# Optimization experiments

Hardware: AMD Instinct MI355X
Metric: run time of the kernel (lower is better)

Reference implementation:

```python
import jax, jax.numpy as jnp
import numpy as np

T, B, I, H, L = 512, 256, 128, 256, 2

def _gru_layer(x, W_ih, W_hh, b_ih, b_hh):
    # x: [T, B, in], W_ih: [3H, in], W_hh: [3H, H], biases: [3H]
    # PyTorch gate order: r, z, n
    Hd = W_hh.shape[1]
    gi = jnp.einsum('tbi,gi->tbg', x, W_ih) + b_ih  # precompute input gates [T,B,3H]

    def step(h, gi_t):
        gh = h @ W_hh.T + b_hh
        i_r, i_z, i_n = jnp.split(gi_t, 3, axis=-1)
        h_r, h_z, h_n = jnp.split(gh, 3, axis=-1)
        r = jax.nn.sigmoid(i_r + h_r)
        z = jax.nn.sigmoid(i_z + h_z)
        n = jnp.tanh(i_n + r * h_n)
        h_new = (1.0 - z) * n + z * h
        return h_new, h_new

    h0 = jnp.zeros((x.shape[1], Hd), dtype=x.dtype)
    _, hs = jax.lax.scan(step, h0, gi)
    return hs  # [T, B, H]

def setup_inputs() -> dict:
    key = jax.random.key(0)
    ks = jax.random.split(key, 11)
    s = 1.0 / np.sqrt(H)
    u = lambda k, shp: jax.random.uniform(k, shp, jnp.float32, -s, s)
    return {
        'x': jax.random.normal(ks[0], (T, B, I), jnp.float32),
        'W_ih0': u(ks[1], (3 * H, I)),
        'W_hh0': u(ks[2], (3 * H, H)),
        'b_ih0': u(ks[3], (3 * H,)),
        'b_hh0': u(ks[4], (3 * H,)),
        'W_ih1': u(ks[5], (3 * H, H)),
        'W_hh1': u(ks[6], (3 * H, H)),
        'b_ih1': u(ks[7], (3 * H,)),
        'b_hh1': u(ks[8], (3 * H,)),
        'W_fc': u(ks[9], (H, H)),
        'b_fc': u(ks[10], (H,)),
    }

def reference(x, W_ih0, W_hh0, b_ih0, b_hh0, W_ih1, W_hh1, b_ih1, b_hh1, W_fc, b_fc):
    h1 = _gru_layer(x, W_ih0, W_hh0, b_ih0, b_hh0)   # [T,B,H]
    h2 = _gru_layer(h1, W_ih1, W_hh1, b_ih1, b_hh1)  # [T,B,H]
    last = h2[-1]                                    # [B,H] last timestep
    return last @ W_fc.T + b_fc
```

## Files before the change

kernel.cpp:

```cpp
#include <hip/hip_runtime.h>

#define TT 512
#define BB 256
#define II 128
#define HH 256
#define LDH 264

typedef __attribute__((ext_vector_type(8))) short short8;
typedef __attribute__((ext_vector_type(4))) float floatx4;
typedef __attribute__((ext_vector_type(4))) float fvec4;
typedef unsigned long long u64;

#define OFF_WIH0 0
#define OFF_WHH0 (OFF_WIH0 + 3 * HH * II)
#define OFF_WIH1 (OFF_WHH0 + 3 * HH * HH)
#define OFF_WHH1 (OFF_WIH1 + 3 * HH * HH)
#define W_TOTAL (OFF_WHH1 + 3 * HH * HH)
#define H1G_OFF W_TOTAL
#define H2G_OFF (H1G_OFF + 2 * BB * HH)
#define WS_SHORTS (H2G_OFF + 2 * BB * HH)
#define FLAGS_OFF_BYTES (WS_SHORTS * 2)
#define FLAG_STRIDE 32

__device__ __forceinline__ short f2bf(float f) {
  unsigned u = __builtin_bit_cast(unsigned, f);
  u = u + 0x7fffu + ((u >> 16) & 1u);
  return (short)(u >> 16);
}
__device__ __forceinline__ float fast_sigmoid(float x) {
  return __fdividef(1.0f, 1.0f + __expf(-x));
}
__device__ __forceinline__ float fast_tanh(float x) {
  return 1.0f - __fdividef(2.0f, 1.0f + __expf(2.0f * x));
}
__device__ __forceinline__ short8 cvt8(const float* __restrict__ p) {
  fvec4 lo = *(const fvec4*)p;
  fvec4 hi = *(const fvec4*)(p + 4);
  short8 r;
  r[0] = f2bf(lo[0]); r[1] = f2bf(lo[1]); r[2] = f2bf(lo[2]); r[3] = f2bf(lo[3]);
  r[4] = f2bf(hi[0]); r[5] = f2bf(hi[1]); r[6] = f2bf(hi[2]); r[7] = f2bf(hi[3]);
  return r;
}
__device__ __forceinline__ u64 ld_sc1(const u64* p) {
  return __hip_atomic_load(p, __ATOMIC_RELAXED, __HIP_MEMORY_SCOPE_AGENT);
}

__global__ __launch_bounds__(256) void cvt_weights(
    const float* __restrict__ w0, const float* __restrict__ w1,
    const float* __restrict__ w2, const float* __restrict__ w3,
    short* __restrict__ out) {
  int i = blockIdx.x * 256 + threadIdx.x;
  if (i >= W_TOTAL) return;
  float v;
  if (i < OFF_WHH0)      v = w0[i - OFF_WIH0];
  else if (i < OFF_WIH1) v = w1[i - OFF_WHH0];
  else if (i < OFF_WHH1) v = w2[i - OFF_WIH1];
  else                   v = w3[i - OFF_WHH1];
  out[i] = f2bf(v);
}

__global__ __launch_bounds__(256) void init_state(unsigned* __restrict__ hz,
                                                  unsigned* __restrict__ flags) {
  int i = blockIdx.x * 256 + threadIdx.x;
  if (i < 2 * BB * HH) hz[i] = 0u;
  if (i < 16 * FLAG_STRIDE) flags[i] = 0u;
}

__global__ __launch_bounds__(384) void gru_sync(
    const float* __restrict__ x, const short* __restrict__ wb,
    const float* __restrict__ bih0, const float* __restrict__ bhh0,
    const float* __restrict__ bih1, const float* __restrict__ bhh1,
    const float* __restrict__ Wfc, const float* __restrict__ bfc,
    short* __restrict__ h1g, short* __restrict__ h2g,
    unsigned* __restrict__ flags, float* __restrict__ out) {
  const int tid = threadIdx.x;
  const int lane = tid & 63;
  const int w = tid >> 6;
  const int quad = lane >> 4;
  const int col = lane & 15;
  const int bt = blockIdx.x & 15;
  const int ht = blockIdx.x >> 4;
  const int layer = w / 3, gate = w % 3;
  const int j = ht * 16 + col;

  __shared__ __align__(16) short ldsA[2][16][LDH];
  __shared__ __align__(16) float gt[2][6][16][20];

  const short* wih = wb + (layer ? OFF_WIH1 : OFF_WIH0);
  const short* whh = wb + (layer ? OFF_WHH1 : OFF_WHH0);
  short8 wfI[8], wfH[8];
  if (layer == 0) {
#pragma unroll
    for (int f = 0; f < 4; ++f)
      wfI[f] = *(const short8*)(wih + (gate * HH + j) * II + f * 32 + quad * 8);
#pragma unroll
    for (int f = 4; f < 8; ++f) wfI[f] = short8{0, 0, 0, 0, 0, 0, 0, 0};
  } else {
#pragma unroll
    for (int f = 0; f < 8; ++f)
      wfI[f] = *(const short8*)(wih + (gate * HH + j) * HH + f * 32 + quad * 8);
  }
#pragma unroll
  for (int f = 0; f < 8; ++f)
    wfH[f] = *(const short8*)(whh + (gate * HH + j) * HH + f * 32 + quad * 8);

  const float* bihL = layer ? bih1 : bih0;
  const float* bhhL = layer ? bhh1 : bhh0;
  float bI, bH;
  if (gate == 2) { bI = bihL[2 * HH + j]; bH = bhhL[2 * HH + j]; }
  else { bI = bihL[gate * HH + j] + bhhL[gate * HH + j]; bH = 0.f; }

  float h1a = 0.f, h1b = 0.f, h2a = 0.f, h2b = 0.f;
  const int r1 = tid >> 3, c1 = (tid & 7) * 2;
  const int r2 = (tid - 256) >> 3, c2 = ((tid - 256) & 7) * 2;

  unsigned* cnt = flags + bt * FLAG_STRIDE;
  const size_t tbase = (size_t)(bt * 16) * HH;

  for (int p = 0; p <= TT; ++p) {
    short8 ax[4];
    if (w < 3 && p < TT) {
      const float* xr = x + ((size_t)p * BB + bt * 16 + col) * II + quad * 8;
#pragma unroll
      for (int f = 0; f < 4; ++f) ax[f] = cvt8(xr + f * 32);
    }

    if (p > 0) {
      if (tid == 0) {
        unsigned tgt = 16u * (unsigned)p;
        int guard = 0;
        while (__hip_atomic_load(cnt, __ATOMIC_RELAXED,
                                 __HIP_MEMORY_SCOPE_AGENT) < tgt &&
               guard < (1 << 20))
          ++guard;
      }
      __syncthreads();
    }

    {
      const u64* s1 = (const u64*)(h1g + ((p + 1) & 1) * BB * HH + tbase);
      const u64* s2 = (const u64*)(h2g + (p & 1) * BB * HH + tbase);
      u64* d1 = (u64*)&ldsA[0][0][0];
      u64* d2 = (u64*)&ldsA[1][0][0];
      if (tid < 256) {
#pragma unroll
        for (int q = 0; q < 4; ++q) {
          int i = tid * 4 + q, row = i >> 6, c = i & 63;
          d1[row * (LDH / 4) + c] = ld_sc1(s1 + i);
        }
      }
      if (tid >= 128) {
        int t2 = tid - 128;
#pragma unroll
        for (int q = 0; q < 4; ++q) {
          int i = t2 * 4 + q, row = i >> 6, c = i & 63;
          d2[row * (LDH / 4) + c] = ld_sc1(s2 + i);
        }
      }
    }
    __syncthreads();

    floatx4 aI = floatx4{bI, bI, bI, bI};
    floatx4 aH = floatx4{bH, bH, bH, bH};
    const short* a1 = &ldsA[0][col][0];
    const short* a2 = &ldsA[1][col][0];
    if (layer == 0) {
      if (p < TT) {
#pragma unroll
        for (int f = 0; f < 4; ++f)
          aI = __builtin_amdgcn_mfma_f32_16x16x32_bf16(ax[f], wfI[f], aI, 0, 0, 0);
      }
#pragma unroll
      for (int f = 0; f < 8; ++f) {
        short8 a = *(const short8*)(a1 + f * 32 + quad * 8);
        aH = __builtin_amdgcn_mfma_f32_16x16x32_bf16(a, wfH[f], aH, 0, 0, 0);
      }
    } else {
#pragma unroll
      for (int f = 0; f < 8; ++f) {
        short8 a = *(const short8*)(a1 + f * 32 + quad * 8);
        aI = __builtin_amdgcn_mfma_f32_16x16x32_bf16(a, wfI[f], aI, 0, 0, 0);
      }
#pragma unroll
      for (int f = 0; f < 8; ++f) {
        short8 a = *(const short8*)(a2 + f * 32 + quad * 8);
        aH = __builtin_amdgcn_mfma_f32_16x16x32_bf16(a, wfH[f], aH, 0, 0, 0);
      }
    }
#pragma unroll
    for (int i = 0; i < 4; ++i) {
      gt[0][w][quad * 4 + i][col] = aI[i];
      gt[1][w][quad * 4 + i][col] = aH[i];
    }
    __syncthreads();

    if (tid < 128 && p < TT) {
      float rA = fast_sigmoid(gt[0][0][r1][c1] + gt[1][0][r1][c1]);
      float zA = fast_sigmoid(gt[0][1][r1][c1] + gt[1][1][r1][c1]);
      float nA = fast_tanh(gt[0][2][r1][c1] + rA * gt[1][2][r1][c1]);
      h1a = nA + zA * (h1a - nA);
      float rB = fast_sigmoid(gt[0][0][r1][c1 + 1] + gt[1][0][r1][c1 + 1]);
      float zB = fast_sigmoid(gt[0][1][r1][c1 + 1] + gt[1][1][r1][c1 + 1]);
      float nB = fast_tanh(gt[0][2][r1][c1 + 1] + rB * gt[1][2][r1][c1 + 1]);
      h1b = nB + zB * (h1b - nB);
      unsigned val = ((unsigned)(unsigned short)f2bf(h1b) << 16) |
                     (unsigned)(unsigned short)f2bf(h1a);
      unsigned* dst = (unsigned*)(h1g + (p & 1) * BB * HH +
                                  (bt * 16 + r1) * HH + ht * 16 + c1);
      __hip_atomic_store(dst, val, __ATOMIC_RELAXED, __HIP_MEMORY_SCOPE_AGENT);
    }
    if (tid >= 256 && p > 0) {
      float rA = fast_sigmoid(gt[0][3][r2][c2] + gt[1][3][r2][c2]);
      float zA = fast_sigmoid(gt[0][4][r2][c2] + gt[1][4][r2][c2]);
      float nA = fast_tanh(gt[0][5][r2][c2] + rA * gt[1][5][r2][c2]);
      h2a = nA + zA * (h2a - nA);
      float rB = fast_sigmoid(gt[0][3][r2][c2 + 1] + gt[1][3][r2][c2 + 1]);
      float zB = fast_sigmoid(gt[0][4][r2][c2 + 1] + gt[1][4][r2][c2 + 1]);
      float nB = fast_tanh(gt[0][5][r2][c2 + 1] + rB * gt[1][5][r2][c2 + 1]);
      h2b = nB + zB * (h2b - nB);
      unsigned val = ((unsigned)(unsigned short)f2bf(h2b) << 16) |
                     (unsigned)(unsigned short)f2bf(h2a);
      unsigned* dst = (unsigned*)(h2g + ((p + 1) & 1) * BB * HH +
                                  (bt * 16 + r2) * HH + ht * 16 + c2);
      __hip_atomic_store(dst, val, __ATOMIC_RELAXED, __HIP_MEMORY_SCOPE_AGENT);
    }
    __syncthreads();
    if (tid == 0)
      __hip_atomic_fetch_add(cnt, 1u, __ATOMIC_RELAXED,
                             __HIP_MEMORY_SCOPE_AGENT);
  }

  if (tid == 0) {
    unsigned tgt = 16u * (unsigned)(TT + 1);
    int guard = 0;
    while (__hip_atomic_load(cnt, __ATOMIC_RELAXED, __HIP_MEMORY_SCOPE_AGENT) <
               tgt &&
           guard < (1 << 20))
      ++guard;
  }
  __syncthreads();
  {
    const u64* s1 = (const u64*)(h2g + 1 * BB * HH + tbase);
    u64* d1 = (u64*)&ldsA[0][0][0];
    if (tid < 256) {
#pragma unroll
      for (int q = 0; q < 4; ++q) {
        int i = tid * 4 + q, row = i >> 6, c = i & 63;
        d1[row * (LDH / 4) + c] = ld_sc1(s1 + i);
      }
    }
  }
  __syncthreads();
  if (w == 0) {
    float bbv = bfc[j];
    floatx4 acc = floatx4{bbv, bbv, bbv, bbv};
#pragma unroll
    for (int f = 0; f < 8; ++f) {
      short8 a = *(const short8*)(&ldsA[0][col][0] + f * 32 + quad * 8);
      short8 bfrag = cvt8(Wfc + j * HH + f * 32 + quad * 8);
      acc = __builtin_amdgcn_mfma_f32_16x16x32_bf16(a, bfrag, acc, 0, 0, 0);
    }
#pragma unroll
    for (int i = 0; i < 4; ++i)
      out[(size_t)(bt * 16 + quad * 4 + i) * HH + j] = acc[i];
  }
}

extern "C" void kernel_launch(void* const* d_in, const int* in_sizes, int n_in,
                              void* d_out, int out_size, void* d_ws,
                              size_t ws_size, hipStream_t stream) {
  const float* x = (const float*)d_in[0];
  const float* Wih0 = (const float*)d_in[1];
  const float* Whh0 = (const float*)d_in[2];
  const float* bih0 = (const float*)d_in[3];
  const float* bhh0 = (const float*)d_in[4];
  const float* Wih1 = (const float*)d_in[5];
  const float* Whh1 = (const float*)d_in[6];
  const float* bih1 = (const float*)d_in[7];
  const float* bhh1 = (const float*)d_in[8];
  const float* Wfc = (const float*)d_in[9];
  const float* bfc = (const float*)d_in[10];

  short* wb = (short*)d_ws;
  short* h1g = wb + H1G_OFF;
  short* h2g = wb + H2G_OFF;
  unsigned* flags = (unsigned*)((char*)d_ws + FLAGS_OFF_BYTES);
  unsigned* hz = (unsigned*)(wb + H1G_OFF);

  cvt_weights<<<(W_TOTAL + 255) / 256, 256, 0, stream>>>(Wih0, Whh0, Wih1, Whh1, wb);
  init_state<<<(2 * BB * HH + 255) / 256, 256, 0, stream>>>(hz, flags);
  gru_sync<<<256, 384, 0, stream>>>(x, wb, bih0, bhh0, bih1, bhh1, Wfc, bfc,
                                    h1g, h2g, flags, (float*)d_out);
}
```

Before: 1.891 ms.

## Process two batch tiles per block to reuse register-held weights

```diff
diff --git a/kernel.cpp b/kernel.cpp
--- a/kernel.cpp
+++ b/kernel.cpp
@@ -78,13 +78,13 @@
   const int w = tid >> 6;
   const int quad = lane >> 4;
   const int col = lane & 15;
-  const int bt = blockIdx.x & 15;
-  const int ht = blockIdx.x >> 4;
+  const int q = blockIdx.x & 7;
+  const int ht = blockIdx.x >> 3;
   const int layer = w / 3, gate = w % 3;
   const int j = ht * 16 + col;
 
-  __shared__ __align__(16) short ldsA[2][16][LDH];
-  __shared__ __align__(16) float gt[2][6][16][20];
+  __shared__ __align__(16) short lds[2][2][16][LDH];
+  __shared__ __align__(16) float gt[2][2][6][16][20];
 
   const short* wih = wb + (layer ? OFF_WIH1 : OFF_WIH0);
   const short* whh = wb + (layer ? OFF_WHH1 : OFF_WHH0);
@@ -110,19 +110,25 @@
   if (gate == 2) { bI = bihL[2 * HH + j]; bH = bhhL[2 * HH + j]; }
   else { bI = bihL[gate * HH + j] + bhhL[gate * HH + j]; bH = 0.f; }
 
-  float h1a = 0.f, h1b = 0.f, h2a = 0.f, h2b = 0.f;
+  float h1aA = 0.f, h1bA = 0.f, h2aA = 0.f, h2bA = 0.f;
+  float h1aB = 0.f, h1bB = 0.f, h2aB = 0.f, h2bB = 0.f;
   const int r1 = tid >> 3, c1 = (tid & 7) * 2;
   const int r2 = (tid - 256) >> 3, c2 = ((tid - 256) & 7) * 2;
 
-  unsigned* cnt = flags + bt * FLAG_STRIDE;
-  const size_t tbase = (size_t)(bt * 16) * HH;
+  unsigned* cnt = flags + q * FLAG_STRIDE;
+  const size_t tbaseA = (size_t)(q * 16) * HH;
+  const size_t tbaseB = (size_t)((q + 8) * 16) * HH;
 
   for (int p = 0; p <= TT; ++p) {
-    short8 ax[4];
+    short8 axA[4], axB[4];
     if (w < 3 && p < TT) {
-      const float* xr = x + ((size_t)p * BB + bt * 16 + col) * II + quad * 8;
-#pragma unroll
-      for (int f = 0; f < 4; ++f) ax[f] = cvt8(xr + f * 32);
+      const float* xrA = x + ((size_t)p * BB + q * 16 + col) * II + quad * 8;
+      const float* xrB = xrA + (size_t)8 * 16 * II;
+#pragma unroll
+      for (int f = 0; f < 4; ++f) {
+        axA[f] = cvt8(xrA + f * 32);
+        axB[f] = cvt8(xrB + f * 32);
+      }
     }
 
     if (p > 0) {
@@ -138,91 +144,145 @@
     }
 
     {
-      const u64* s1 = (const u64*)(h1g + ((p + 1) & 1) * BB * HH + tbase);
-      const u64* s2 = (const u64*)(h2g + (p & 1) * BB * HH + tbase);
-      u64* d1 = (u64*)&ldsA[0][0][0];
-      u64* d2 = (u64*)&ldsA[1][0][0];
+      const u64* s1A = (const u64*)(h1g + ((p + 1) & 1) * BB * HH + tbaseA);
+      const u64* s2A = (const u64*)(h2g + (p & 1) * BB * HH + tbaseA);
+      const u64* s1B = (const u64*)(h1g + ((p + 1) & 1) * BB * HH + tbaseB);
+      const u64* s2B = (const u64*)(h2g + (p & 1) * BB * HH + tbaseB);
+      u64* d1A = (u64*)&lds[0][0][0][0];
+      u64* d2A = (u64*)&lds[0][1][0][0];
+      u64* d1B = (u64*)&lds[1][0][0][0];
+      u64* d2B = (u64*)&lds[1][1][0][0];
       if (tid < 256) {
 #pragma unroll
-        for (int q = 0; q < 4; ++q) {
-          int i = tid * 4 + q, row = i >> 6, c = i & 63;
-          d1[row * (LDH / 4) + c] = ld_sc1(s1 + i);
+        for (int qq = 0; qq < 4; ++qq) {
+          int i = tid * 4 + qq, row = i >> 6, c = i & 63;
+          d1A[row * (LDH / 4) + c] = ld_sc1(s1A + i);
+          d1B[row * (LDH / 4) + c] = ld_sc1(s1B + i);
         }
       }
       if (tid >= 128) {
         int t2 = tid - 128;
 #pragma unroll
-        for (int q = 0; q < 4; ++q) {
-          int i = t2 * 4 + q, row = i >> 6, c = i & 63;
-          d2[row * (LDH / 4) + c] = ld_sc1(s2 + i);
+        for (int qq = 0; qq < 4; ++qq) {
+          int i = t2 * 4 + qq, row = i >> 6, c = i & 63;
+          d2A[row * (LDH / 4) + c] = ld_sc1(s2A + i);
+          d2B[row * (LDH / 4) + c] = ld_sc1(s2B + i);
         }
       }
     }
     __syncthreads();
 
-    floatx4 aI = floatx4{bI, bI, bI, bI};
-    floatx4 aH = floatx4{bH, bH, bH, bH};
-    const short* a1 = &ldsA[0][col][0];
-    const short* a2 = &ldsA[1][col][0];
+    floatx4 aIA = floatx4{bI, bI, bI, bI};
+    floatx4 aHA = floatx4{bH, bH, bH, bH};
+    floatx4 aIB = floatx4{bI, bI, bI, bI};
+    floatx4 aHB = floatx4{bH, bH, bH, bH};
+    const short* a1A = &lds[0][0][col][0];
+    const short* a2A = &lds[0][1][col][0];
+    const short* a1B = &lds[1][0][col][0];
+    const short* a2B = &lds[1][1][col][0];
     if (layer == 0) {
       if (p < TT) {
 #pragma unroll
-        for (int f = 0; f < 4; ++f)
-          aI = __builtin_amdgcn_mfma_f32_16x16x32_bf16(ax[f], wfI[f], aI, 0, 0, 0);
+        for (int f = 0; f < 4; ++f) {
+          aIA = __builtin_amdgcn_mfma_f32_16x16x32_bf16(axA[f], wfI[f], aIA, 0, 0, 0);
+          aIB = __builtin_amdgcn_mfma_f32_16x16x32_bf16(axB[f], wfI[f], aIB, 0, 0, 0);
+        }
       }
 #pragma unroll
       for (int f = 0; f < 8; ++f) {
-        short8 a = *(const short8*)(a1 + f * 32 + quad * 8);
-        aH = __builtin_amdgcn_mfma_f32_16x16x32_bf16(a, wfH[f], aH, 0, 0, 0);
+        short8 aA = *(const short8*)(a1A + f * 32 + quad * 8);
+        short8 aB = *(const short8*)(a1B + f * 32 + quad * 8);
+        aHA = __builtin_amdgcn_mfma_f32_16x16x32_bf16(aA, wfH[f], aHA, 0, 0, 0);
+        aHB = __builtin_amdgcn_mfma_f32_16x16x32_bf16(aB, wfH[f], aHB, 0, 0, 0);
       }
     } else {
 #pragma unroll
       for (int f = 0; f < 8; ++f) {
-        short8 a = *(const short8*)(a1 + f * 32 + quad * 8);
-        aI = __builtin_amdgcn_mfma_f32_16x16x32_bf16(a, wfI[f], aI, 0, 0, 0);
+        short8 aA = *(const short8*)(a1A + f * 32 + quad * 8);
+        short8 aB = *(const short8*)(a1B + f * 32 + quad * 8);
+        aIA = __builtin_amdgcn_mfma_f32_16x16x32_bf16(aA, wfI[f], aIA, 0, 0, 0);
+        aIB = __builtin_amdgcn_mfma_f32_16x16x32_bf16(aB, wfI[f], aIB, 0, 0, 0);
       }
 #pragma unroll
       for (int f = 0; f < 8; ++f) {
-        short8 a = *(const short8*)(a2 + f * 32 + quad * 8);
-        aH = __builtin_amdgcn_mfma_f32_16x16x32_bf16(a, wfH[f], aH, 0, 0, 0);
+        short8 aA = *(const short8*)(a2A + f * 32 + quad * 8);
+        short8 aB = *(const short8*)(a2B + f * 32 + quad * 8);
+        aHA = __builtin_amdgcn_mfma_f32_16x16x32_bf16(aA, wfH[f], aHA, 0, 0, 0);
+        aHB = __builtin_amdgcn_mfma_f32_16x16x32_bf16(aB, wfH[f], aHB, 0, 0, 0);
       }
     }
 #pragma unroll
     for (int i = 0; i < 4; ++i) {
-      gt[0][w][quad * 4 + i][col] = aI[i];
-      gt[1][w][quad * 4 + i][col] = aH[i];
+      gt[0][0][w][quad * 4 + i][col] = aIA[i];
+      gt[0][1][w][quad * 4 + i][col] = aHA[i];
+      gt[1][0][w][quad * 4 + i][col] = aIB[i];
+      gt[1][1][w][quad * 4 + i][col] = aHB[i];
     }
     __syncthreads();
 
     if (tid < 128 && p < TT) {
-      float rA = fast_sigmoid(gt[0][0][r1][c1] + gt[1][0][r1][c1]);
-      float zA = fast_sigmoid(gt[0][1][r1][c1] + gt[1][1][r1][c1]);
-      float nA = fast_tanh(gt[0][2][r1][c1] + rA * gt[1][2][r1][c1]);
-      h1a = nA + zA * (h1a - nA);
-      float rB = fast_sigmoid(gt[0][0][r1][c1 + 1] + gt[1][0][r1][c1 + 1]);
-      float zB = fast_sigmoid(gt[0][1][r1][c1 + 1] + gt[1][1][r1][c1 + 1]);
-      float nB = fast_tanh(gt[0][2][r1][c1 + 1] + rB * gt[1][2][r1][c1 + 1]);
-      h1b = nB + zB * (h1b - nB);
-      unsigned val = ((unsigned)(unsigned short)f2bf(h1b) << 16) |
-                     (unsigned)(unsigned short)f2bf(h1a);
-      unsigned* dst = (unsigned*)(h1g + (p & 1) * BB * HH +
-                                  (bt * 16 + r1) * HH + ht * 16 + c1);
-      __hip_atomic_store(dst, val, __ATOMIC_RELAXED, __HIP_MEMORY_SCOPE_AGENT);
+      {
+        float rA = fast_sigmoid(gt[0][0][0][r1][c1] + gt[0][1][0][r1][c1]);
+        float zA = fast_sigmoid(gt[0][0][1][r1][c1] + gt[0][1][1][r1][c1]);
+        float nA = fast_tanh(gt[0][0][2][r1][c1] + rA * gt[0][1][2][r1][c1]);
+        h1aA = nA + zA * (h1aA - nA);
+        float rB = fast_sigmoid(gt[0][0][0][r1][c1 + 1] + gt[0][1][0][r1][c1 + 1]);
+        float zB = fast_sigmoid(gt[0][0][1][r1][c1 + 1] + gt[0][1][1][r1][c1 + 1]);
+        float nB = fast_tanh(gt[0][0][2][r1][c1 + 1] + rB * gt[0][1][2][r1][c1 + 1]);
+        h1bA = nB + zB * (h1bA - nB);
+        unsigned val = ((unsigned)(unsigned short)f2bf(h1bA) << 16) |
+                       (unsigned)(unsigned short)f2bf(h1aA);
+        unsigned* dst = (unsigned*)(h1g + (p & 1) * BB * HH +
+                                    (q * 16 + r1) * HH + ht * 16 + c1);
+        __hip_atomic_store(dst, val, __ATOMIC_RELAXED, __HIP_MEMORY_SCOPE_AGENT);
+      }
+      {
+        float rA = fast_sigmoid(gt[1][0][0][r1][c1] + gt[1][1][0][r1][c1]);
+        float zA = fast_sigmoid(gt[1][0][1][r1][c1] + gt[1][1][1][r1][c1]);
+        float nA = fast_tanh(gt[1][0][2][r1][c1] + rA * gt[1][1][2][r1][c1]);
+        h1aB = nA + zA * (h1aB - nA);
+        float rB = fast_sigmoid(gt[1][0][0][r1][c1 + 1] + gt[1][1][0][r1][c1 + 1]);
+        float zB = fast_sigmoid(gt[1][0][1][r1][c1 + 1] + gt[1][1][1][r1][c1 + 1]);
+        float nB = fast_tanh(gt[1][0][2][r1][c1 + 1] + rB * gt[1][1][2][r1][c1 + 1]);
+        h1bB = nB + zB * (h1bB - nB);
+        unsigned val = ((unsigned)(unsigned short)f2bf(h1bB) << 16) |
+                       (unsigned)(unsigned short)f2bf(h1aB);
+        unsigned* dst = (unsigned*)(h1g + (p & 1) * BB * HH +
+                                    ((q + 8) * 16 + r1) * HH + ht * 16 + c1);
+        __hip_atomic_store(dst, val, __ATOMIC_RELAXED, __HIP_MEMORY_SCOPE_AGENT);
+      }
     }
     if (tid >= 256 && p > 0) {
-      float rA = fast_sigmoid(gt[0][3][r2][c2] + gt[1][3][r2][c2]);
-      float zA = fast_sigmoid(gt[0][4][r2][c2] + gt[1][4][r2][c2]);
-      float nA = fast_tanh(gt[0][5][r2][c2] + rA * gt[1][5][r2][c2]);
-      h2a = nA + zA * (h2a - nA);
-      float rB = fast_sigmoid(gt[0][3][r2][c2 + 1] + gt[1][3][r2][c2 + 1]);
-      float zB = fast_sigmoid(gt[0][4][r2][c2 + 1] + gt[1][4][r2][c2 + 1]);
-      float nB = fast_tanh(gt[0][5][r2][c2 + 1] + rB * gt[1][5][r2][c2 + 1]);
-      h2b = nB + zB * (h2b - nB);
-      unsigned val = ((unsigned)(unsigned short)f2bf(h2b) << 16) |
-                     (unsigned)(unsigned short)f2bf(h2a);
-      unsigned* dst = (unsigned*)(h2g + ((p + 1) & 1) * BB * HH +
-                                  (bt * 16 + r2) * HH + ht * 16 + c2);
-      __hip_atomic_store(dst, val, __ATOMIC_RELAXED, __HIP_MEMORY_SCOPE_AGENT);
+      {
+        float rA = fast_sigmoid(gt[0][0][3][r2][c2] + gt[0][1][3][r2][c2]);
+        float zA = fast_sigmoid(gt[0][0][4][r2][c2] + gt[0][1][4][r2][c2]);
+        float nA = fast_tanh(gt[0][0][5][r2][c2] + rA * gt[0][1][5][r2][c2]);
+        h2aA = nA + zA * (h2aA - nA);
+        float rB = fast_sigmoid(gt[0][0][3][r2][c2 + 1] + gt[0][1][3][r2][c2 + 1]);
+        float zB = fast_sigmoid(gt[0][0][4][r2][c2 + 1] + gt[0][1][4][r2][c2 + 1]);
+        float nB = fast_tanh(gt[0][0][5][r2][c2 + 1] + rB * gt[0][1][5][r2][c2 + 1]);
+        h2bA = nB + zB * (h2bA - nB);
+        unsigned val = ((unsigned)(unsigned short)f2bf(h2bA) << 16) |
+                       (unsigned)(unsigned short)f2bf(h2aA);
+        unsigned* dst = (unsigned*)(h2g + ((p + 1) & 1) * BB * HH +
+                                    (q * 16 + r2) * HH + ht * 16 + c2);
+        __hip_atomic_store(dst, val, __ATOMIC_RELAXED, __HIP_MEMORY_SCOPE_AGENT);
+      }
+      {
+        float rA = fast_sigmoid(gt[1][0][3][r2][c2] + gt[1][1][3][r2][c2]);
+        float zA = fast_sigmoid(gt[1][0][4][r2][c2] + gt[1][1][4][r2][c2]);
+        float nA = fast_tanh(gt[1][0][5][r2][c2] + rA * gt[1][1][5][r2][c2]);
+        h2aB = nA + zA * (h2aB - nA);
+        float rB = fast_sigmoid(gt[1][0][3][r2][c2 + 1] + gt[1][1][3][r2][c2 + 1]);
+        float zB = fast_sigmoid(gt[1][0][4][r2][c2 + 1] + gt[1][1][4][r2][c2 + 1]);
+        float nB = fast_tanh(gt[1][0][5][r2][c2 + 1] + rB * gt[1][1][5][r2][c2 + 1]);
+        h2bB = nB + zB * (h2bB - nB);
+        unsigned val = ((unsigned)(unsigned short)f2bf(h2bB) << 16) |
+                       (unsigned)(unsigned short)f2bf(h2aB);
+        unsigned* dst = (unsigned*)(h2g + ((p + 1) & 1) * BB * HH +
+                                    ((q + 8) * 16 + r2) * HH + ht * 16 + c2);
+        __hip_atomic_store(dst, val, __ATOMIC_RELAXED, __HIP_MEMORY_SCOPE_AGENT);
+      }
     }
     __syncthreads();
     if (tid == 0)
@@ -240,29 +300,35 @@
   }
   __syncthreads();
   {
-    const u64* s1 = (const u64*)(h2g + 1 * BB * HH + tbase);
-    u64* d1 = (u64*)&ldsA[0][0][0];
+    const u64* sA = (const u64*)(h2g + 1 * BB * HH + tbaseA);
+    const u64* sB = (const u64*)(h2g + 1 * BB * HH + tbaseB);
+    u64* dA = (u64*)&lds[0][0][0][0];
+    u64* dB = (u64*)&lds[1][0][0][0];
     if (tid < 256) {
 #pragma unroll
-      for (int q = 0; q < 4; ++q) {
-        int i = tid * 4 + q, row = i >> 6, c = i & 63;
-        d1[row * (LDH / 4) + c] = ld_sc1(s1 + i);
+      for (int qq = 0; qq < 4; ++qq) {
+        int i = tid * 4 + qq, row = i >> 6, c = i & 63;
+        dA[row * (LDH / 4) + c] = ld_sc1(sA + i);
+        dB[row * (LDH / 4) + c] = ld_sc1(sB + i);
       }
     }
   }
   __syncthreads();
-  if (w == 0) {
+  if (w < 2) {
+    const int g = w;
+    const short* av = &lds[g][0][col][0];
     float bbv = bfc[j];
     floatx4 acc = floatx4{bbv, bbv, bbv, bbv};
 #pragma unroll
     for (int f = 0; f < 8; ++f) {
-      short8 a = *(const short8*)(&ldsA[0][col][0] + f * 32 + quad * 8);
+      short8 a = *(const short8*)(av + f * 32 + quad * 8);
       short8 bfrag = cvt8(Wfc + j * HH + f * 32 + quad * 8);
       acc = __builtin_amdgcn_mfma_f32_16x16x32_bf16(a, bfrag, acc, 0, 0, 0);
     }
+    const int brow = (g ? (q + 8) : q) * 16;
 #pragma unroll
     for (int i = 0; i < 4; ++i)
-      out[(size_t)(bt * 16 + quad * 4 + i) * HH + j] = acc[i];
+      out[(size_t)(brow + quad * 4 + i) * HH + j] = acc[i];
   }
 }
 
@@ -289,6 +355,6 @@
 
   cvt_weights<<<(W_TOTAL + 255) / 256, 256, 0, stream>>>(Wih0, Whh0, Wih1, Whh1, wb);
   init_state<<<(2 * BB * HH + 255) / 256, 256, 0, stream>>>(hz, flags);
-  gru_sync<<<256, 384, 0, stream>>>(x, wb, bih0, bhh0, bih1, bhh1, Wfc, bfc,
+  gru_sync<<<128, 384, 0, stream>>>(x, wb, bih0, bhh0, bih1, bhh1, Wfc, bfc,
                                     h1g, h2g, flags, (float*)d_out);
 }
```

Result: slower. 3.303 ms (+74.6%).

## Split GRU into single-wave blocks per layer with per-tile flag dataflow sync

Applied to the files above, without the earlier changes.

```diff
diff --git a/kernel.cpp b/kernel.cpp
--- a/kernel.cpp
+++ b/kernel.cpp
@@ -4,7 +4,6 @@
 #define BB 256
 #define II 128
 #define HH 256
-#define LDH 264
 
 typedef __attribute__((ext_vector_type(8))) short short8;
 typedef __attribute__((ext_vector_type(4))) float floatx4;
@@ -21,6 +20,9 @@
 #define WS_SHORTS (H2G_OFF + 2 * BB * HH)
 #define FLAGS_OFF_BYTES (WS_SHORTS * 2)
 #define FLAG_STRIDE 32
+#define HPARW (BB * HH / 4)
+
+struct U64x2 { u64 lo, hi; };
 
 __device__ __forceinline__ short f2bf(float f) {
   unsigned u = __builtin_bit_cast(unsigned, f);
@@ -44,6 +46,16 @@
 __device__ __forceinline__ u64 ld_sc1(const u64* p) {
   return __hip_atomic_load(p, __ATOMIC_RELAXED, __HIP_MEMORY_SCOPE_AGENT);
 }
+__device__ __forceinline__ unsigned ld_flag(const unsigned* p) {
+  return __hip_atomic_load(p, __ATOMIC_RELAXED, __HIP_MEMORY_SCOPE_AGENT);
+}
+__device__ __forceinline__ void st_flag(unsigned* p, unsigned v) {
+  __hip_atomic_store(p, v, __ATOMIC_RELAXED, __HIP_MEMORY_SCOPE_AGENT);
+}
+__device__ __forceinline__ void st_h(unsigned short* p, unsigned short v) {
+  __hip_atomic_store(p, v, __ATOMIC_RELAXED, __HIP_MEMORY_SCOPE_AGENT);
+}
+#define DRAIN_VMEM asm volatile("s_waitcnt vmcnt(0)" ::: "memory")
 
 __global__ __launch_bounds__(256) void cvt_weights(
     const float* __restrict__ w0, const float* __restrict__ w1,
@@ -63,200 +75,187 @@
                                                   unsigned* __restrict__ flags) {
   int i = blockIdx.x * 256 + threadIdx.x;
   if (i < 2 * BB * HH) hz[i] = 0u;
-  if (i < 16 * FLAG_STRIDE) flags[i] = 0u;
-}
-
-__global__ __launch_bounds__(384) void gru_sync(
+  if (i < 32 * FLAG_STRIDE) flags[i] = 0u;
+}
+
+__global__ __launch_bounds__(64) void gru_sync(
     const float* __restrict__ x, const short* __restrict__ wb,
     const float* __restrict__ bih0, const float* __restrict__ bhh0,
     const float* __restrict__ bih1, const float* __restrict__ bhh1,
     const float* __restrict__ Wfc, const float* __restrict__ bfc,
     short* __restrict__ h1g, short* __restrict__ h2g,
     unsigned* __restrict__ flags, float* __restrict__ out) {
-  const int tid = threadIdx.x;
-  const int lane = tid & 63;
-  const int w = tid >> 6;
+  const int lane = threadIdx.x;
   const int quad = lane >> 4;
   const int col = lane & 15;
-  const int bt = blockIdx.x & 15;
-  const int ht = blockIdx.x >> 4;
-  const int layer = w / 3, gate = w % 3;
+  const int bid = blockIdx.x;
+  const int layer = bid >> 8;
+  const int bt = (bid >> 4) & 15;
+  const int ht = bid & 15;
   const int j = ht * 16 + col;
 
-  __shared__ __align__(16) short ldsA[2][16][LDH];
-  __shared__ __align__(16) float gt[2][6][16][20];
+  unsigned* h1fl = flags + bt * FLAG_STRIDE;
+  unsigned* h2fl = flags + (16 + bt) * FLAG_STRIDE;
+  unsigned* myfl = layer ? h2fl : h1fl;
 
   const short* wih = wb + (layer ? OFF_WIH1 : OFF_WIH0);
   const short* whh = wb + (layer ? OFF_WHH1 : OFF_WHH0);
-  short8 wfI[8], wfH[8];
-  if (layer == 0) {
-#pragma unroll
-    for (int f = 0; f < 4; ++f)
-      wfI[f] = *(const short8*)(wih + (gate * HH + j) * II + f * 32 + quad * 8);
-#pragma unroll
-    for (int f = 4; f < 8; ++f) wfI[f] = short8{0, 0, 0, 0, 0, 0, 0, 0};
-  } else {
-#pragma unroll
-    for (int f = 0; f < 8; ++f)
-      wfI[f] = *(const short8*)(wih + (gate * HH + j) * HH + f * 32 + quad * 8);
+  const int KI = layer ? HH : II;
+  short8 wI0[8], wI1[8], wI2[8], wH0[8], wH1[8], wH2[8];
+#pragma unroll
+  for (int f = 0; f < 8; ++f) {
+    if (f * 32 < KI) {
+      wI0[f] = *(const short8*)(wih + (0 * HH + j) * KI + f * 32 + quad * 8);
+      wI1[f] = *(const short8*)(wih + (1 * HH + j) * KI + f * 32 + quad * 8);
+      wI2[f] = *(const short8*)(wih + (2 * HH + j) * KI + f * 32 + quad * 8);
+    } else {
+      wI0[f] = short8{0,0,0,0,0,0,0,0};
+      wI1[f] = short8{0,0,0,0,0,0,0,0};
+      wI2[f] = short8{0,0,0,0,0,0,0,0};
+    }
+    wH0[f] = *(const short8*)(whh + (0 * HH + j) * HH + f * 32 + quad * 8);
+    wH1[f] = *(const short8*)(whh + (1 * HH + j) * HH + f * 32 + quad * 8);
+    wH2[f] = *(const short8*)(whh + (2 * HH + j) * HH + f * 32 + quad * 8);
   }
-#pragma unroll
-  for (int f = 0; f < 8; ++f)
-    wfH[f] = *(const short8*)(whh + (gate * HH + j) * HH + f * 32 + quad * 8);
-
   const float* bihL = layer ? bih1 : bih0;
   const float* bhhL = layer ? bhh1 : bhh0;
-  float bI, bH;
-  if (gate == 2) { bI = bihL[2 * HH + j]; bH = bhhL[2 * HH + j]; }
-  else { bI = bihL[gate * HH + j] + bhhL[gate * HH + j]; bH = 0.f; }
-
-  float h1a = 0.f, h1b = 0.f, h2a = 0.f, h2b = 0.f;
-  const int r1 = tid >> 3, c1 = (tid & 7) * 2;
-  const int r2 = (tid - 256) >> 3, c2 = ((tid - 256) & 7) * 2;
-
-  unsigned* cnt = flags + bt * FLAG_STRIDE;
-  const size_t tbase = (size_t)(bt * 16) * HH;
-
-  for (int p = 0; p <= TT; ++p) {
+  const float bI0 = bihL[j] + bhhL[j];
+  const float bI1 = bihL[HH + j] + bhhL[HH + j];
+  const float bI2 = bihL[2 * HH + j];
+  const float bH2 = bhhL[2 * HH + j];
+
+  float hprev0 = 0.f, hprev1 = 0.f, hprev2 = 0.f, hprev3 = 0.f;
+
+  const u64* h1w = (const u64*)h1g;
+  const u64* h2w = (const u64*)h2g;
+  const int rowW = (bt * 16 + col) * 64;
+
+  for (int p = 0; p < TT; ++p) {
     short8 ax[4];
-    if (w < 3 && p < TT) {
+    if (layer == 0) {
       const float* xr = x + ((size_t)p * BB + bt * 16 + col) * II + quad * 8;
 #pragma unroll
       for (int f = 0; f < 4; ++f) ax[f] = cvt8(xr + f * 32);
     }
 
-    if (p > 0) {
-      if (tid == 0) {
-        unsigned tgt = 16u * (unsigned)p;
+    {
+      unsigned tgt = 0;
+      const unsigned* fp = h1fl;
+      if (layer == 0) {
+        if (lane < 16)      { tgt = (unsigned)p; fp = h1fl + lane; }
+        else if (lane < 32) { tgt = (p >= 1) ? (unsigned)(p - 1) : 0u; fp = h2fl + (lane - 16); }
+      } else {
+        if (lane < 16)      { tgt = (unsigned)p; fp = h2fl + lane; }
+        else if (lane < 32) { tgt = (unsigned)(p + 1); fp = h1fl + (lane - 16); }
+      }
+      if (layer == 1 || p > 0) {
         int guard = 0;
-        while (__hip_atomic_load(cnt, __ATOMIC_RELAXED,
-                                 __HIP_MEMORY_SCOPE_AGENT) < tgt &&
-               guard < (1 << 20))
-          ++guard;
-      }
-      __syncthreads();
-    }
-
+        for (;;) {
+          unsigned v = ld_flag(fp);
+          if (__all(v >= tgt) || ++guard > (1 << 20)) break;
+        }
+      }
+    }
+
+    short8 a1[8], a2[8];
+    if (layer == 0) {
+      const u64* s1 = h1w + ((p + 1) & 1) * HPARW + rowW;
+#pragma unroll
+      for (int f = 0; f < 8; ++f) {
+        u64 lo = ld_sc1(s1 + f * 8 + quad * 2);
+        u64 hi = ld_sc1(s1 + f * 8 + quad * 2 + 1);
+        a1[f] = __builtin_bit_cast(short8, U64x2{lo, hi});
+      }
+    } else {
+      const u64* s1 = h1w + (p & 1) * HPARW + rowW;
+      const u64* s2 = h2w + ((p + 1) & 1) * HPARW + rowW;
+#pragma unroll
+      for (int f = 0; f < 8; ++f) {
+        u64 lo = ld_sc1(s1 + f * 8 + quad * 2);
+        u64 hi = ld_sc1(s1 + f * 8 + quad * 2 + 1);
+        a1[f] = __builtin_bit_cast(short8, U64x2{lo, hi});
+      }
+#pragma unroll
+      for (int f = 0; f < 8; ++f) {
+        u64 lo = ld_sc1(s2 + f * 8 + quad * 2);
+        u64 hi = ld_sc1(s2 + f * 8 + quad * 2 + 1);
+        a2[f] = __builtin_bit_cast(short8, U64x2{lo, hi});
+      }
+    }
+
+    floatx4 aR = floatx4{bI0, bI0, bI0, bI0};
+    floatx4 aZ = floatx4{bI1, bI1, bI1, bI1};
+    floatx4 aN = floatx4{bI2, bI2, bI2, bI2};
+    floatx4 hN = floatx4{bH2, bH2, bH2, bH2};
+    if (layer == 0) {
+#pragma unroll
+      for (int f = 0; f < 4; ++f) {
+        aR = __builtin_amdgcn_mfma_f32_16x16x32_bf16(ax[f], wI0[f], aR, 0, 0, 0);
+        aZ = __builtin_amdgcn_mfma_f32_16x16x32_bf16(ax[f], wI1[f], aZ, 0, 0, 0);
+        aN = __builtin_amdgcn_mfma_f32_16x16x32_bf16(ax[f], wI2[f], aN, 0, 0, 0);
+      }
+#pragma unroll
+      for (int f = 0; f < 8; ++f) {
+        aR = __builtin_amdgcn_mfma_f32_16x16x32_bf16(a1[f], wH0[f], aR, 0, 0, 0);
+        aZ = __builtin_amdgcn_mfma_f32_16x16x32_bf16(a1[f], wH1[f], aZ, 0, 0, 0);
+        hN = __builtin_amdgcn_mfma_f32_16x16x32_bf16(a1[f], wH2[f], hN, 0, 0, 0);
+      }
+    } else {
+#pragma unroll
+      for (int f = 0; f < 8; ++f) {
+        aR = __builtin_amdgcn_mfma_f32_16x16x32_bf16(a1[f], wI0[f], aR, 0, 0, 0);
+        aZ = __builtin_amdgcn_mfma_f32_16x16x32_bf16(a1[f], wI1[f], aZ, 0, 0, 0);
+        aN = __builtin_amdgcn_mfma_f32_16x16x32_bf16(a1[f], wI2[f], aN, 0, 0, 0);
+      }
+#pragma unroll
+      for (int f = 0; f < 8; ++f) {
+        aR = __builtin_amdgcn_mfma_f32_16x16x32_bf16(a2[f], wH0[f], aR, 0, 0, 0);
+        aZ = __builtin_amdgcn_mfma_f32_16x16x32_bf16(a2[f], wH1[f], aZ, 0, 0, 0);
+        hN = __builtin_amdgcn_mfma_f32_16x16x32_bf16(a2[f], wH2[f], hN, 0, 0, 0);
+      }
+    }
+
+    short* hout = (layer ? h2g : h1g) + (p & 1) * BB * HH;
+    unsigned short* dst = (unsigned short*)hout +
+                          (size_t)(bt * 16 + quad * 4) * HH + j;
     {
-      const u64* s1 = (const u64*)(h1g + ((p + 1) & 1) * BB * HH + tbase);
-      const u64* s2 = (const u64*)(h2g + (p & 1) * BB * HH + tbase);
-      u64* d1 = (u64*)&ldsA[0][0][0];
-      u64* d2 = (u64*)&ldsA[1][0][0];
-      if (tid < 256) {
-#pragma unroll
-        for (int q = 0; q < 4; ++q) {
-          int i = tid * 4 + q, row = i >> 6, c = i & 63;
-          d1[row * (LDH / 4) + c] = ld_sc1(s1 + i);
-        }
-      }
-      if (tid >= 128) {
-        int t2 = tid - 128;
-#pragma unroll
-        for (int q = 0; q < 4; ++q) {
-          int i = t2 * 4 + q, row = i >> 6, c = i & 63;
-          d2[row * (LDH / 4) + c] = ld_sc1(s2 + i);
-        }
-      }
-    }
-    __syncthreads();
-
-    floatx4 aI = floatx4{bI, bI, bI, bI};
-    floatx4 aH = floatx4{bH, bH, bH, bH};
-    const short* a1 = &ldsA[0][col][0];
-    const short* a2 = &ldsA[1][col][0];
-    if (layer == 0) {
-      if (p < TT) {
-#pragma unroll
-        for (int f = 0; f < 4; ++f)
-          aI = __builtin_amdgcn_mfma_f32_16x16x32_bf16(ax[f], wfI[f], aI, 0, 0, 0);
-      }
-#pragma unroll
-      for (int f = 0; f < 8; ++f) {
-        short8 a = *(const short8*)(a1 + f * 32 + quad * 8);
-        aH = __builtin_amdgcn_mfma_f32_16x16x32_bf16(a, wfH[f], aH, 0, 0, 0);
-      }
-    } else {
-#pragma unroll
-      for (int f = 0; f < 8; ++f) {
-        short8 a = *(const short8*)(a1 + f * 32 + quad * 8);
-        aI = __builtin_amdgcn_mfma_f32_16x16x32_bf16(a, wfI[f], aI, 0, 0, 0);
-      }
-#pragma unroll
-      for (int f = 0; f < 8; ++f) {
-        short8 a = *(const short8*)(a2 + f * 32 + quad * 8);
-        aH = __builtin_amdgcn_mfma_f32_16x16x32_bf16(a, wfH[f], aH, 0, 0, 0);
-      }
-    }
-#pragma unroll
-    for (int i = 0; i < 4; ++i) {
-      gt[0][w][quad * 4 + i][col] = aI[i];
-      gt[1][w][quad * 4 + i][col] = aH[i];
-    }
-    __syncthreads();
-
-    if (tid < 128 && p < TT) {
-      float rA = fast_sigmoid(gt[0][0][r1][c1] + gt[1][0][r1][c1]);
-      float zA = fast_sigmoid(gt[0][1][r1][c1] + gt[1][1][r1][c1]);
-      float nA = fast_tanh(gt[0][2][r1][c1] + rA * gt[1][2][r1][c1]);
-      h1a = nA + zA * (h1a - nA);
-      float rB = fast_sigmoid(gt[0][0][r1][c1 + 1] + gt[1][0][r1][c1 + 1]);
-      float zB = fast_sigmoid(gt[0][1][r1][c1 + 1] + gt[1][1][r1][c1 + 1]);
-      float nB = fast_tanh(gt[0][2][r1][c1 + 1] + rB * gt[1][2][r1][c1 + 1]);
-      h1b = nB + zB * (h1b - nB);
-      unsigned val = ((unsigned)(unsigned short)f2bf(h1b) << 16) |
-                     (unsigned)(unsigned short)f2bf(h1a);
-      unsigned* dst = (unsigned*)(h1g + (p & 1) * BB * HH +
-                                  (bt * 16 + r1) * HH + ht * 16 + c1);
-      __hip_atomic_store(dst, val, __ATOMIC_RELAXED, __HIP_MEMORY_SCOPE_AGENT);
-    }
-    if (tid >= 256 && p > 0) {
-      float rA = fast_sigmoid(gt[0][3][r2][c2] + gt[1][3][r2][c2]);
-      float zA = fast_sigmoid(gt[0][4][r2][c2] + gt[1][4][r2][c2]);
-      float nA = fast_tanh(gt[0][5][r2][c2] + rA * gt[1][5][r2][c2]);
-      h2a = nA + zA * (h2a - nA);
-      float rB = fast_sigmoid(gt[0][3][r2][c2 + 1] + gt[1][3][r2][c2 + 1]);
-      float zB = fast_sigmoid(gt[0][4][r2][c2 + 1] + gt[1][4][r2][c2 + 1]);
-      float nB = fast_tanh(gt[0][5][r2][c2 + 1] + rB * gt[1][5][r2][c2 + 1]);
-      h2b = nB + zB * (h2b - nB);
-      unsigned val = ((unsigned)(unsigned short)f2bf(h2b) << 16) |
-                     (unsigned)(unsigned short)f2bf(h2a);
-      unsigned* dst = (unsigned*)(h2g + ((p + 1) & 1) * BB * HH +
-                                  (bt * 16 + r2) * HH + ht * 16 + c2);
-      __hip_atomic_store(dst, val, __ATOMIC_RELAXED, __HIP_MEMORY_SCOPE_AGENT);
-    }
-    __syncthreads();
-    if (tid == 0)
-      __hip_atomic_fetch_add(cnt, 1u, __ATOMIC_RELAXED,
-                             __HIP_MEMORY_SCOPE_AGENT);
+      float r0 = fast_sigmoid(aR[0]), z0 = fast_sigmoid(aZ[0]);
+      float n0 = fast_tanh(aN[0] + r0 * hN[0]);
+      hprev0 = n0 + z0 * (hprev0 - n0);
+      st_h(dst + 0 * HH, (unsigned short)f2bf(hprev0));
+      float r1 = fast_sigmoid(aR[1]), z1 = fast_sigmoid(aZ[1]);
+      float n1 = fast_tanh(aN[1] + r1 * hN[1]);
+      hprev1 = n1 + z1 * (hprev1 - n1);
+      st_h(dst + 1 * HH, (unsigned short)f2bf(hprev1));
+      float r2 = fast_sigmoid(aR[2]), z2 = fast_sigmoid(aZ[2]);
+      float n2 = fast_tanh(aN[2] + r2 * hN[2]);
+      hprev2 = n2 + z2 * (hprev2 - n2);
+      st_h(dst + 2 * HH, (unsigned short)f2bf(hprev2));
+      float r3 = fast_sigmoid(aR[3]), z3 = fast_sigmoid(aZ[3]);
+      float n3 = fast_tanh(aN[3] + r3 * hN[3]);
+      hprev3 = n3 + z3 * (hprev3 - n3);
+      st_h(dst + 3 * HH, (unsigned short)f2bf(hprev3));
+    }
+    DRAIN_VMEM;
+    if (lane == 0) st_flag(myfl + ht, (unsigned)(p + 1));
   }
 
-  if (tid == 0) {
-    unsigned tgt = 16u * (unsigned)(TT + 1);
-    int guard = 0;
-    while (__hip_atomic_load(cnt, __ATOMIC_RELAXED, __HIP_MEMORY_SCOPE_AGENT) <
-               tgt &&
-           guard < (1 << 20))
-      ++guard;
-  }
-  __syncthreads();
-  {
-    const u64* s1 = (const u64*)(h2g + 1 * BB * HH + tbase);
-    u64* d1 = (u64*)&ldsA[0][0][0];
-    if (tid < 256) {
-#pragma unroll
-      for (int q = 0; q < 4; ++q) {
-        int i = tid * 4 + q, row = i >> 6, c = i & 63;
-        d1[row * (LDH / 4) + c] = ld_sc1(s1 + i);
-      }
-    }
-  }
-  __syncthreads();
-  if (w == 0) {
+  if (layer == 1) {
+    {
+      int guard = 0;
+      for (;;) {
+        unsigned v = (lane < 16) ? ld_flag(h2fl + lane) : (unsigned)TT;
+        if (__all(v >= (unsigned)TT) || ++guard > (1 << 20)) break;
+      }
+    }
+    const u64* s2 = h2w + ((TT - 1) & 1) * HPARW + rowW;
     float bbv = bfc[j];
     floatx4 acc = floatx4{bbv, bbv, bbv, bbv};
 #pragma unroll
     for (int f = 0; f < 8; ++f) {
-      short8 a = *(const short8*)(&ldsA[0][col][0] + f * 32 + quad * 8);
+      u64 lo = ld_sc1(s2 + f * 8 + quad * 2);
+      u64 hi = ld_sc1(s2 + f * 8 + quad * 2 + 1);
+      short8 a = __builtin_bit_cast(short8, U64x2{lo, hi});
       short8 bfrag = cvt8(Wfc + j * HH + f * 32 + quad * 8);
       acc = __builtin_amdgcn_mfma_f32_16x16x32_bf16(a, bfrag, acc, 0, 0, 0);
     }
@@ -289,6 +288,6 @@
 
   cvt_weights<<<(W_TOTAL + 255) / 256, 256, 0, stream>>>(Wih0, Whh0, Wih1, Whh1, wb);
   init_state<<<(2 * BB * HH + 255) / 256, 256, 0, stream>>>(hz, flags);
-  gru_sync<<<256, 384, 0, stream>>>(x, wb, bih0, bhh0, bih1, bhh1, Wfc, bfc,
-                                    h1g, h2g, flags, (float*)d_out);
-}
+  gru_sync<<<512, 64, 0, stream>>>(x, wb, bih0, bhh0, bih1, bhh1, Wfc, bfc,
+                                   h1g, h2g, flags, (float*)d_out);
+}
```

Result: slower. 2.093 ms (+10.7%).
